# Kernel tuning notes

Measured on AMD Instinct MI355X. Metric: run time of the kernel, lower is better.

Reference implementation:

```python
import jax, jax.numpy as jnp
import numpy as np

N = 20000   # nodes
E = 40000   # directed edges
F_IN = 13   # dataset.num_features
G = 1000    # graphs in batch
DIMS = [(13, 32), (32, 64), (64, 64)]  # (M_in, M_out) per NNConv layer


def setup_inputs() -> dict:
    key = jax.random.key(0)
    ks = list(jax.random.split(key, 32))
    inp = {}
    inp["x"] = jax.random.normal(ks[0], (N, F_IN), jnp.float32)
    inp["edge_index"] = jax.random.randint(ks[1], (2, E), 0, N, dtype=jnp.int32)
    inp["edge_attr"] = jax.random.uniform(ks[2], (E, 5), dtype=jnp.float32)
    inp["batch"] = jnp.sort(jax.random.randint(ks[3], (N,), 0, G, dtype=jnp.int32))
    i = 4
    for l, (mi, mo) in enumerate(DIMS):
        inp[f"w1_{l}"] = jax.random.normal(ks[i], (5, 128), jnp.float32) / np.sqrt(5.0).astype(np.float32); i += 1
        inp[f"b1_{l}"] = jnp.zeros((128,), jnp.float32)
        inp[f"w2_{l}"] = jax.random.normal(ks[i], (128, mi * mo), jnp.float32) / np.sqrt(128.0).astype(np.float32); i += 1
        inp[f"b2_{l}"] = jnp.zeros((mi * mo,), jnp.float32)
        inp[f"root_{l}"] = jax.random.normal(ks[i], (mi, mo), jnp.float32) / np.sqrt(float(mi)).astype(np.float32); i += 1
        inp[f"bias_{l}"] = jnp.zeros((mo,), jnp.float32)
    inp["fc1_w"] = jax.random.normal(ks[i], (64, 32), jnp.float32) / 8.0; i += 1
    inp["fc1_b"] = jnp.zeros((32,), jnp.float32)
    inp["fc2_w"] = jax.random.normal(ks[i], (32, 16), jnp.float32) / np.sqrt(32.0).astype(np.float32); i += 1
    inp["fc2_b"] = jnp.zeros((16,), jnp.float32)
    inp["fc3_w"] = jax.random.normal(ks[i], (16, 1), jnp.float32) / 4.0; i += 1
    inp["fc3_b"] = jnp.zeros((1,), jnp.float32)
    return inp


def _nnconv(x, src, dst, edge_attr, w1, b1, w2, b2, root, bias, mi, mo):
    # edge MLP: [E,5] -> [E,128] -> [E, mi*mo] per-edge weight matrices
    h = jax.nn.relu(edge_attr @ w1 + b1)
    We = (h @ w2 + b2).reshape(-1, mi, mo)          # [E, mi, mo]
    msg = jnp.einsum('ei,eio->eo', x[src], We)      # gather + per-edge matmul
    agg = jax.ops.segment_sum(msg, dst, num_segments=x.shape[0])  # scatter-add
    return x @ root + agg + bias                    # NNConv root weight + bias


def _forward(x, edge_index, edge_attr, batch, convs, fc1_w, fc1_b, fc2_w, fc2_b, fc3_w, fc3_b):
    src, dst = edge_index[0], edge_index[1]
    for (mi, mo), (w1, b1, w2, b2, root, bias) in zip(DIMS, convs):
        x = jax.nn.elu(_nnconv(x, src, dst, edge_attr, w1, b1, w2, b2, root, bias, mi, mo))
    # scatter_mean pooling over graphs
    sums = jax.ops.segment_sum(x, batch, num_segments=G)
    cnt = jax.ops.segment_sum(jnp.ones((x.shape[0],), x.dtype), batch, num_segments=G)
    xg = sums / jnp.maximum(cnt, 1.0)[:, None]
    xg = jax.nn.elu(xg @ fc1_w + fc1_b)
    xg = jax.nn.elu(xg @ fc2_w + fc2_b)
    return (xg @ fc3_w + fc3_b).reshape(-1)


def reference(x, edge_index, edge_attr, batch,
              w1_0, b1_0, w2_0, b2_0, root_0, bias_0,
              w1_1, b1_1, w2_1, b2_1, root_1, bias_1,
              w1_2, b1_2, w2_2, b2_2, root_2, bias_2,
              fc1_w, fc1_b, fc2_w, fc2_b, fc3_w, fc3_b):
    convs = [(w1_0, b1_0, w2_0, b2_0, root_0, bias_0),
             (w1_1, b1_1, w2_1, b2_1, root_1, bias_1),
             (w1_2, b1_2, w2_2, b2_2, root_2, bias_2)]
    return _forward(x, edge_index, edge_attr, batch, convs,
                    fc1_w, fc1_b, fc2_w, fc2_b, fc3_w, fc3_b)
```

## Files before the change

### kernel.cpp

```cpp
#include <hip/hip_runtime.h>
#include <stdint.h>
#include <math.h>

typedef _Float16 half8_t __attribute__((ext_vector_type(8)));
typedef float floatx4 __attribute__((ext_vector_type(4)));

#define NN 20000
#define NE 40000
#define NG 1000
#define NBLK 313
#define NSPLIT 4

__global__ __launch_bounds__(256) void prep_fused_kernel(
    const float* __restrict__ x, _Float16* __restrict__ e16,
    const float* __restrict__ w2a, const float* __restrict__ b2a, _Float16* __restrict__ oa,
    const float* __restrict__ w2b, const float* __restrict__ b2b, _Float16* __restrict__ ob,
    const float* __restrict__ w2c, const float* __restrict__ b2c, _Float16* __restrict__ oc,
    int* __restrict__ deg)
{
  if (blockIdx.x < 1250) {
    int idx = blockIdx.x * 256 + threadIdx.x;
    int n = idx >> 4, i = idx & 15;
    e16[idx] = (i < 13) ? (_Float16)x[(size_t)n * 13 + i] : (_Float16)0.f;
    return;
  }
  if (blockIdx.x >= 1680) {
    int n = (blockIdx.x - 1680) * 256 + threadIdx.x;
    if (n < NN) deg[n] = 0;
    return;
  }
  const int TOT0 = 68 * 2 * 64, TOT1 = 132 * 4 * 64, TOT2 = 264 * 4 * 64;
  int idx = (blockIdx.x - 1250) * 256 + threadIdx.x;
  const float *w2, *b2; _Float16* op; int mi, mo, mpsh, CT;
  if (idx < TOT0) { w2 = w2a; b2 = b2a; op = oa; mi = 13; mo = 32; mpsh = 4; CT = 2; }
  else if (idx < TOT0 + TOT1) { idx -= TOT0; w2 = w2b; b2 = b2b; op = ob; mi = 32; mo = 64; mpsh = 5; CT = 4; }
  else if (idx < TOT0 + TOT1 + TOT2) { idx -= TOT0 + TOT1; w2 = w2c; b2 = b2c; op = oc; mi = 64; mo = 64; mpsh = 6; CT = 4; }
  else return;
  int l = idx & 63;
  int ct = (idx >> 6) % CT;
  int c = idx / (64 * CT);
  int q = l >> 4;
  int n = ct * 16 + (l & 15);
  int mask = (1 << mpsh) - 1;
  half8_t v;
#pragma unroll
  for (int j = 0; j < 8; ++j) {
    int r = c * 32 + q * 8 + j;
    int k = r >> mpsh, i = r & mask;
    float f = 0.f;
    if (i < mi) {
      if (k < 128) f = w2[(size_t)(k * mi + i) * mo + n];
      else if (k == 128) f = b2[(size_t)i * mo + n];
    }
    v[j] = (_Float16)f;
  }
  *(half8_t*)(op + (size_t)idx * 8) = v;
}

__global__ __launch_bounds__(256) void deg_kernel(const int* __restrict__ dst, int* __restrict__ deg) {
  int e = blockIdx.x * 256 + threadIdx.x;
  if (e < NE) atomicAdd(&deg[dst[e]], 1);
}

__global__ __launch_bounds__(1024) void scan_kernel(
    const int* __restrict__ deg, int* __restrict__ row_ptr, int* __restrict__ cursor)
{
  constexpr int CH = 20;
  __shared__ int wsum[16];
  int t = threadIdx.x;
  int lane = t & 63, w = t >> 6;
  int base = t * CH;
  int local[CH];
#pragma unroll
  for (int i = 0; i < CH; ++i) {
    int n = base + i;
    local[i] = (n < NN) ? deg[n] : 0;
  }
  int s = 0;
#pragma unroll
  for (int i = 0; i < CH; ++i) s += local[i];
  int sc = s;
#pragma unroll
  for (int d = 1; d < 64; d <<= 1) {
    int v = __shfl_up(sc, d, 64);
    if (lane >= d) sc += v;
  }
  if (lane == 63) wsum[w] = sc;
  __syncthreads();
  if (w == 0 && lane < 16) {
    int v = wsum[lane];
    int scc = v;
#pragma unroll
    for (int d = 1; d < 16; d <<= 1) {
      int u = __shfl_up(scc, d, 64);
      if (lane >= d) scc += u;
    }
    wsum[lane] = scc - v;
  }
  __syncthreads();
  int run = wsum[w] + (sc - s);
#pragma unroll
  for (int i = 0; i < CH; ++i) {
    int n = base + i;
    if (n < NN) { row_ptr[n] = run; cursor[n] = run; run += local[i]; }
    else if (n == NN) row_ptr[NN] = run;
  }
}

__global__ __launch_bounds__(256) void fill_kernel(
    const int* __restrict__ dst, int* __restrict__ cursor, int* __restrict__ eids)
{
  int e = blockIdx.x * 256 + threadIdx.x;
  if (e < NE) { int p = atomicAdd(&cursor[dst[e]], 1); eids[p] = e; }
}

template <int MIP, int MO, int NCC, int KCNT>
__global__ __launch_bounds__(256, 4) void msg9_kernel(
    const float* __restrict__ ea, const float* __restrict__ w1,
    const float* __restrict__ b1, const _Float16* __restrict__ xe,
    const int* __restrict__ src,
    const _Float16* __restrict__ w2h, _Float16* __restrict__ msgp)
{
  constexpr int EPB = 128;
  constexpr int CT = MO / 16;
  constexpr int CHB = CT * 1024;
  constexpr int XV = (MIP == 64) ? 2 : 1;
  constexpr int KH = (KCNT + 1) >> 1;

  __shared__ uint4 wsb[2][CHB / 16];
  __shared__ _Float16 h16[KCNT * EPB];
  __shared__ float w1s[5 * 128 + 128];

  const int t = threadIdx.x;
  const int wave = t >> 6, lane = t & 63;
  const int l15 = lane & 15, q = lane >> 4;
  const int split = blockIdx.x / NBLK;
  const int e0 = (blockIdx.x % NBLK) * EPB;
  const int c0 = NCC * split;
  const int kg0 = KCNT * split;

  const char* wgp = (const char*)w2h + (size_t)c0 * CHB;
  uint4 ra4, rb4; uint2 ra2, rb2;
  if constexpr (CT == 4) {
    ra4 = *(const uint4*)(wgp + t * 16);
    rb4 = *(const uint4*)(wgp + CHB + t * 16);
  } else {
    ra2 = *(const uint2*)(wgp + t * 8);
    rb2 = *(const uint2*)(wgp + CHB + t * 8);
  }

  const int wbase = wave * 32;
  half8_t xf[2][XV];
#pragma unroll
  for (int s = 0; s < 2; ++s) {
    int eg = e0 + wbase + s * 16 + l15; if (eg >= NE) eg = NE - 1;
    const _Float16* xr = xe + (size_t)src[eg] * MIP;
    int i0 = (MIP == 16) ? (q & 1) * 8 : q * 8;
    xf[s][0] = *(const half8_t*)(xr + i0);
    if constexpr (MIP == 64)
      xf[s][XV - 1] = *(const half8_t*)(xr + 32 + q * 8);
  }

  const int te = t & 127;
  float ear[5];
  {
    int eg = e0 + te; if (eg >= NE) eg = NE - 1;
#pragma unroll
    for (int j = 0; j < 5; ++j) ear[j] = ea[(size_t)eg * 5 + j];
  }
  for (int i = t; i < 768; i += 256) w1s[i] = (i < 640) ? w1[i] : b1[i - 640];
  __syncthreads();

  {
    int kh = t >> 7;
    int klo = kh * KH;
    int khi = klo + KH; if (khi > KCNT) khi = KCNT;
    for (int kl = klo; kl < khi; ++kl) {
      int kg = kg0 + kl;
      float v;
      if (kg < 128) {
        v = w1s[640 + kg];
#pragma unroll
        for (int j = 0; j < 5; ++j) v = fmaf(ear[j], w1s[j * 128 + kg], v);
        v = fmaxf(v, 0.f);
      } else v = (kg == 128) ? 1.f : 0.f;
      h16[kl * EPB + te] = (_Float16)v;
    }
  }
  __syncthreads();

  floatx4 acc[2][CT];
#pragma unroll
  for (int s = 0; s < 2; ++s)
#pragma unroll
    for (int b = 0; b < CT; ++b) acc[s][b] = (floatx4){0.f, 0.f, 0.f, 0.f};

#pragma unroll 2
  for (int cc = 0; cc < NCC; ++cc) {
    const bool odd = (cc & 1) != 0;
    if constexpr (CT == 4) wsb[cc & 1][t] = odd ? rb4 : ra4;
    else ((uint2*)wsb[cc & 1])[t] = odd ? rb2 : ra2;
    if (cc + 2 < NCC) {
      const char* np = wgp + (size_t)(cc + 2) * CHB;
      if constexpr (CT == 4) {
        if (odd) rb4 = *(const uint4*)(np + t * 16); else ra4 = *(const uint4*)(np + t * 16);
      } else {
        if (odd) rb2 = *(const uint2*)(np + t * 8); else ra2 = *(const uint2*)(np + t * 8);
      }
    }
    __syncthreads();
    const _Float16* wb = (const _Float16*)wsb[cc & 1];
    half8_t bf[CT];
#pragma unroll
    for (int b = 0; b < CT; ++b)
      bf[b] = *(const half8_t*)(wb + (b * 64 + lane) * 8);
    int kl;
    if constexpr (MIP == 64) kl = cc >> 1;
    else if constexpr (MIP == 32) kl = cc;
    else kl = 2 * cc + (q >> 1);
#pragma unroll
    for (int s = 0; s < 2; ++s) {
      _Float16 hv = h16[kl * EPB + wbase + s * 16 + l15];
      half8_t af;
      if constexpr (MIP == 64) af = xf[s][cc & 1] * hv;
      else af = xf[s][0] * hv;
#pragma unroll
      for (int b = 0; b < CT; ++b)
        acc[s][b] = __builtin_amdgcn_mfma_f32_16x16x32_f16(af, bf[b], acc[s][b], 0, 0, 0);
    }
  }

  _Float16* mp = msgp + (size_t)split * NE * MO;
#pragma unroll
  for (int s = 0; s < 2; ++s) {
    int rowb = wbase + s * 16 + q * 4;
#pragma unroll
    for (int b = 0; b < CT; ++b) {
      int n = b * 16 + l15;
#pragma unroll
      for (int r = 0; r < 4; ++r) {
        int row = rowb + r;
        int e = e0 + row;
        if (e < NE) mp[(size_t)e * MO + n] = (_Float16)acc[s][b][r];
      }
    }
  }
}

template <int MIP, int NCC, int KCNT>
__global__ __launch_bounds__(256, 4) void msgH_kernel(
    const float* __restrict__ ea, const float* __restrict__ w1,
    const float* __restrict__ b1, const _Float16* __restrict__ xe,
    const int* __restrict__ src,
    const _Float16* __restrict__ w2h, _Float16* __restrict__ msgp)
{
  constexpr int EPB = 128;
  constexpr int MO = 64;
  constexpr int CHB = 4096;
  constexpr int XV = (MIP == 64) ? 2 : 1;
  constexpr int KH = (KCNT + 1) >> 1;

  __shared__ uint4 wsb[2][CHB / 16];
  __shared__ _Float16 h16[KCNT * EPB];
  __shared__ float w1s[5 * 128 + 128];

  const int t = threadIdx.x;
  const int wave = t >> 6, lane = t & 63;
  const int l15 = lane & 15, q = lane >> 4;
  const int mw = wave >> 1;
  const int nw = wave & 1;
  const int split = blockIdx.x / NBLK;
  const int e0 = (blockIdx.x % NBLK) * EPB;
  const int c0 = NCC * split;
  const int kg0 = KCNT * split;

  const char* wgp = (const char*)w2h + (size_t)c0 * CHB;
  uint4 ra4 = *(const uint4*)(wgp + t * 16);
  uint4 rb4 = *(const uint4*)(wgp + CHB + t * 16);

  half8_t xf[4][XV];
#pragma unroll
  for (int s = 0; s < 4; ++s) {
    int eg = e0 + mw * 64 + s * 16 + l15; if (eg >= NE) eg = NE - 1;
    const _Float16* xr = xe + (size_t)src[eg] * MIP;
    xf[s][0] = *(const half8_t*)(xr + q * 8);
    if constexpr (MIP == 64)
      xf[s][XV - 1] = *(const half8_t*)(xr + 32 + q * 8);
  }

  const int te = t & 127;
  float ear[5];
  {
    int eg = e0 + te; if (eg >= NE) eg = NE - 1;
#pragma unroll
    for (int j = 0; j < 5; ++j) ear[j] = ea[(size_t)eg * 5 + j];
  }
  for (int i = t; i < 768; i += 256) w1s[i] = (i < 640) ? w1[i] : b1[i - 640];
  __syncthreads();

  {
    int kh = t >> 7;
    int klo = kh * KH;
    int khi = klo + KH; if (khi > KCNT) khi = KCNT;
    for (int kl = klo; kl < khi; ++kl) {
      int kg = kg0 + kl;
      float v;
      if (kg < 128) {
        v = w1s[640 + kg];
#pragma unroll
        for (int j = 0; j < 5; ++j) v = fmaf(ear[j], w1s[j * 128 + kg], v);
        v = fmaxf(v, 0.f);
      } else v = (kg == 128) ? 1.f : 0.f;
      h16[kl * EPB + te] = (_Float16)v;
    }
  }
  __syncthreads();

  floatx4 acc[4][2];
#pragma unroll
  for (int s = 0; s < 4; ++s)
#pragma unroll
    for (int b = 0; b < 2; ++b) acc[s][b] = (floatx4){0.f, 0.f, 0.f, 0.f};

#pragma unroll 2
  for (int cc = 0; cc < NCC; ++cc) {
    const bool odd = (cc & 1) != 0;
    wsb[cc & 1][t] = odd ? rb4 : ra4;
    if (cc + 2 < NCC) {
      const char* np = wgp + (size_t)(cc + 2) * CHB;
      if (odd) rb4 = *(const uint4*)(np + t * 16); else ra4 = *(const uint4*)(np + t * 16);
    }
    __syncthreads();
    const _Float16* wb = (const _Float16*)wsb[cc & 1];
    half8_t bf[2];
#pragma unroll
    for (int b = 0; b < 2; ++b)
      bf[b] = *(const half8_t*)(wb + ((nw * 2 + b) * 64 + lane) * 8);
    int kl;
    if constexpr (MIP == 64) kl = cc >> 1;
    else kl = cc;
#pragma unroll
    for (int s = 0; s < 4; ++s) {
      _Float16 hv = h16[kl * EPB + mw * 64 + s * 16 + l15];
      half8_t af;
      if constexpr (MIP == 64) af = xf[s][cc & 1] * hv;
      else af = xf[s][0] * hv;
#pragma unroll
      for (int b = 0; b < 2; ++b)
        acc[s][b] = __builtin_amdgcn_mfma_f32_16x16x32_f16(af, bf[b], acc[s][b], 0, 0, 0);
    }
  }

  _Float16* mp = msgp + (size_t)split * NE * MO;
#pragma unroll
  for (int s = 0; s < 4; ++s) {
    int rowb = mw * 64 + s * 16 + q * 4;
#pragma unroll
    for (int b = 0; b < 2; ++b) {
      int n = nw * 32 + b * 16 + l15;
#pragma unroll
      for (int r = 0; r < 4; ++r) {
        int e = e0 + rowb + r;
        if (e < NE) mp[(size_t)e * MO + n] = (_Float16)acc[s][b][r];
      }
    }
  }
}

template <int MIN_, int XST, int MO, int FINAL>
__global__ __launch_bounds__(256) void gather_kernel(
    const _Float16* __restrict__ e16in, const float* __restrict__ root,
    const float* __restrict__ bias, const int* __restrict__ row_ptr,
    const int* __restrict__ eids, const _Float16* __restrict__ msgp,
    _Float16* __restrict__ oute, float* __restrict__ outf)
{
  constexpr int NPB = 256 / MO;
  int n = blockIdx.x * NPB + threadIdx.x / MO;
  int o = threadIdx.x % MO;
  if (n >= NN) return;
  float a = bias[o];
#pragma unroll
  for (int i = 0; i < MIN_; ++i)
    a = fmaf((float)e16in[(size_t)n * XST + i], root[i * MO + o], a);
  int r0 = row_ptr[n], r1 = row_ptr[n + 1];
  for (int j = r0; j < r1; ++j) {
    int e = eids[j];
#pragma unroll
    for (int s = 0; s < NSPLIT; ++s)
      a += (float)msgp[((size_t)s * NE + e) * MO + o];
  }
  if constexpr (FINAL) {
    outf[(size_t)n * MO + o] = a;
  } else {
    float v = a > 0.f ? a : (expf(a) - 1.f);
    oute[(size_t)n * MO + o] = (_Float16)v;
  }
}

__global__ __launch_bounds__(64) void pool_fc_kernel(
    const float* __restrict__ xn2, const int* __restrict__ batch,
    const float* __restrict__ f1w, const float* __restrict__ f1b,
    const float* __restrict__ f2w, const float* __restrict__ f2b,
    const float* __restrict__ f3w, const float* __restrict__ f3b,
    float* __restrict__ out)
{
  __shared__ float xg[64]; __shared__ float a1[32]; __shared__ float a2[16];
  int g = blockIdx.x, t = threadIdx.x;
  int lo = 0, hi = NN;
  while (lo < hi) { int m = (lo + hi) >> 1; if (batch[m] < g) lo = m + 1; else hi = m; }
  int start = lo; hi = NN;
  while (lo < hi) { int m = (lo + hi) >> 1; if (batch[m] <= g) lo = m + 1; else hi = m; }
  int end = lo;
  float acc = 0.f;
  for (int n = start; n < end; ++n) {
    float v = xn2[(size_t)n * 64 + t];
    acc += v > 0.f ? v : (expf(v) - 1.f);
  }
  float c = (end > start) ? (float)(end - start) : 1.f;
  xg[t] = acc / c;
  __syncthreads();
  if (t < 32) {
    float a = f1b[t];
    for (int i = 0; i < 64; ++i) a = fmaf(xg[i], f1w[i * 32 + t], a);
    a1[t] = a > 0.f ? a : (expf(a) - 1.f);
  }
  __syncthreads();
  if (t < 16) {
    float a = f2b[t];
    for (int i = 0; i < 32; ++i) a = fmaf(a1[i], f2w[i * 16 + t], a);
    a2[t] = a > 0.f ? a : (expf(a) - 1.f);
  }
  __syncthreads();
  if (t == 0) {
    float a = f3b[0];
    for (int i = 0; i < 16; ++i) a = fmaf(a2[i], f3w[i], a);
    out[g] = a;
  }
}

extern "C" void kernel_launch(void* const* d_in, const int* in_sizes, int n_in,
                              void* d_out, int out_size, void* d_ws, size_t ws_size,
                              hipStream_t stream)
{
  const float* x_in  = (const float*)d_in[0];
  const int*   ei    = (const int*)d_in[1];
  const float* ea    = (const float*)d_in[2];
  const int*   batch = (const int*)d_in[3];
  const float* W1[3] = {(const float*)d_in[4],  (const float*)d_in[10], (const float*)d_in[16]};
  const float* B1[3] = {(const float*)d_in[5],  (const float*)d_in[11], (const float*)d_in[17]};
  const float* W2[3] = {(const float*)d_in[6],  (const float*)d_in[12], (const float*)d_in[18]};
  const float* B2[3] = {(const float*)d_in[7],  (const float*)d_in[13], (const float*)d_in[19]};
  const float* RT[3] = {(const float*)d_in[8],  (const float*)d_in[14], (const float*)d_in[20]};
  const float* BS[3] = {(const float*)d_in[9],  (const float*)d_in[15], (const float*)d_in[21]};
  const float* f1w = (const float*)d_in[22]; const float* f1b = (const float*)d_in[23];
  const float* f2w = (const float*)d_in[24]; const float* f2b = (const float*)d_in[25];
  const float* f3w = (const float*)d_in[26]; const float* f3b = (const float*)d_in[27];

  char* ws = (char*)d_ws;
  size_t off = 0;
  auto alloc = [&](size_t bytes) { void* p = ws + off; off += (bytes + 255) & ~(size_t)255; return p; };
  float*    xn2   = (float*)alloc((size_t)NN * 64 * 4);
  _Float16* e16_0 = (_Float16*)alloc((size_t)NN * 16 * 2);
  _Float16* e16_1 = (_Float16*)alloc((size_t)NN * 32 * 2);
  _Float16* e16_2 = (_Float16*)alloc((size_t)NN * 64 * 2);
  _Float16* w2h0  = (_Float16*)alloc((size_t)68 * 2048);
  _Float16* w2h1  = (_Float16*)alloc((size_t)132 * 4096);
  _Float16* w2h2  = (_Float16*)alloc((size_t)264 * 4096);
  _Float16* msgp  = (_Float16*)alloc((size_t)NSPLIT * NE * 64 * 2);
  int*      deg     = (int*)alloc((size_t)NN * 4);
  int*      row_ptr = (int*)alloc((size_t)(NN + 1) * 4);
  int*      cursor  = (int*)alloc((size_t)NN * 4);
  int*      eids    = (int*)alloc((size_t)NE * 4);

  const int* srcp = ei;
  const int* dstp = ei + NE;

  prep_fused_kernel<<<1680 + (NN + 255) / 256, 256, 0, stream>>>(
      x_in, e16_0, W2[0], B2[0], w2h0, W2[1], B2[1], w2h1, W2[2], B2[2], w2h2, deg);
  deg_kernel<<<(NE + 255) / 256, 256, 0, stream>>>(dstp, deg);
  scan_kernel<<<1, 1024, 0, stream>>>(deg, row_ptr, cursor);
  fill_kernel<<<(NE + 255) / 256, 256, 0, stream>>>(dstp, cursor, eids);

  msg9_kernel<16, 32, 17, 34><<<NBLK * NSPLIT, 256, 0, stream>>>(
      ea, W1[0], B1[0], e16_0, srcp, w2h0, msgp);
  gather_kernel<13, 16, 32, 0><<<(NN + 7) / 8, 256, 0, stream>>>(
      e16_0, RT[0], BS[0], row_ptr, eids, msgp, e16_1, xn2);

  msgH_kernel<32, 33, 33><<<NBLK * NSPLIT, 256, 0, stream>>>(
      ea, W1[1], B1[1], e16_1, srcp, w2h1, msgp);
  gather_kernel<32, 32, 64, 0><<<(NN + 3) / 4, 256, 0, stream>>>(
      e16_1, RT[1], BS[1], row_ptr, eids, msgp, e16_2, xn2);

  msgH_kernel<64, 66, 33><<<NBLK * NSPLIT, 256, 0, stream>>>(
      ea, W1[2], B1[2], e16_2, srcp, w2h2, msgp);
  gather_kernel<64, 64, 64, 1><<<(NN + 3) / 4, 256, 0, stream>>>(
      e16_2, RT[2], BS[2], row_ptr, eids, msgp, e16_2, xn2);

  pool_fc_kernel<<<NG, 64, 0, stream>>>(xn2, batch, f1w, f1b, f2w, f2b, f3w, f3b, (float*)d_out);
}
```

Before: 297.5 us.

## Process weight chunks in pairs per barrier and give each wave all output columns

```diff
diff --git a/kernel.cpp b/kernel.cpp
--- a/kernel.cpp
+++ b/kernel.cpp
@@ -24,12 +24,12 @@
     e16[idx] = (i < 13) ? (_Float16)x[(size_t)n * 13 + i] : (_Float16)0.f;
     return;
   }
-  if (blockIdx.x >= 1680) {
-    int n = (blockIdx.x - 1680) * 256 + threadIdx.x;
+  if (blockIdx.x >= 1684) {
+    int n = (blockIdx.x - 1684) * 256 + threadIdx.x;
     if (n < NN) deg[n] = 0;
     return;
   }
-  const int TOT0 = 68 * 2 * 64, TOT1 = 132 * 4 * 64, TOT2 = 264 * 4 * 64;
+  const int TOT0 = 68 * 2 * 64, TOT1 = 136 * 4 * 64, TOT2 = 264 * 4 * 64;
   int idx = (blockIdx.x - 1250) * 256 + threadIdx.x;
   const float *w2, *b2; _Float16* op; int mi, mo, mpsh, CT;
   if (idx < TOT0) { w2 = w2a; b2 = b2a; op = oa; mi = 13; mo = 32; mpsh = 4; CT = 2; }
@@ -248,7 +248,7 @@
 }
 
 template <int MIP, int NCC, int KCNT>
-__global__ __launch_bounds__(256, 4) void msgH_kernel(
+__global__ __launch_bounds__(256, 4) void msg9p_kernel(
     const float* __restrict__ ea, const float* __restrict__ w1,
     const float* __restrict__ b1, const _Float16* __restrict__ xe,
     const int* __restrict__ src,
@@ -256,32 +256,35 @@
 {
   constexpr int EPB = 128;
   constexpr int MO = 64;
+  constexpr int CT = 4;
   constexpr int CHB = 4096;
   constexpr int XV = (MIP == 64) ? 2 : 1;
   constexpr int KH = (KCNT + 1) >> 1;
-
-  __shared__ uint4 wsb[2][CHB / 16];
+  static_assert((NCC & 1) == 0, "NCC must be even for paired chunks");
+
+  __shared__ uint4 wsb[2][2][CHB / 16];
   __shared__ _Float16 h16[KCNT * EPB];
   __shared__ float w1s[5 * 128 + 128];
 
   const int t = threadIdx.x;
   const int wave = t >> 6, lane = t & 63;
   const int l15 = lane & 15, q = lane >> 4;
-  const int mw = wave >> 1;
-  const int nw = wave & 1;
   const int split = blockIdx.x / NBLK;
   const int e0 = (blockIdx.x % NBLK) * EPB;
   const int c0 = NCC * split;
   const int kg0 = KCNT * split;
 
   const char* wgp = (const char*)w2h + (size_t)c0 * CHB;
-  uint4 ra4 = *(const uint4*)(wgp + t * 16);
-  uint4 rb4 = *(const uint4*)(wgp + CHB + t * 16);
-
-  half8_t xf[4][XV];
-#pragma unroll
-  for (int s = 0; s < 4; ++s) {
-    int eg = e0 + mw * 64 + s * 16 + l15; if (eg >= NE) eg = NE - 1;
+  uint4 pA0 = *(const uint4*)(wgp + 0 * CHB + t * 16);
+  uint4 pA1 = *(const uint4*)(wgp + 1 * CHB + t * 16);
+  uint4 pB0 = *(const uint4*)(wgp + 2 * CHB + t * 16);
+  uint4 pB1 = *(const uint4*)(wgp + 3 * CHB + t * 16);
+
+  const int wbase = wave * 32;
+  half8_t xf[2][XV];
+#pragma unroll
+  for (int s = 0; s < 2; ++s) {
+    int eg = e0 + wbase + s * 16 + l15; if (eg >= NE) eg = NE - 1;
     const _Float16* xr = xe + (size_t)src[eg] * MIP;
     xf[s][0] = *(const half8_t*)(xr + q * 8);
     if constexpr (MIP == 64)
@@ -316,51 +319,61 @@
   }
   __syncthreads();
 
-  floatx4 acc[4][2];
-#pragma unroll
-  for (int s = 0; s < 4; ++s)
-#pragma unroll
-    for (int b = 0; b < 2; ++b) acc[s][b] = (floatx4){0.f, 0.f, 0.f, 0.f};
+  floatx4 acc[2][CT];
+#pragma unroll
+  for (int s = 0; s < 2; ++s)
+#pragma unroll
+    for (int b = 0; b < CT; ++b) acc[s][b] = (floatx4){0.f, 0.f, 0.f, 0.f};
 
 #pragma unroll 2
-  for (int cc = 0; cc < NCC; ++cc) {
-    const bool odd = (cc & 1) != 0;
-    wsb[cc & 1][t] = odd ? rb4 : ra4;
-    if (cc + 2 < NCC) {
-      const char* np = wgp + (size_t)(cc + 2) * CHB;
-      if (odd) rb4 = *(const uint4*)(np + t * 16); else ra4 = *(const uint4*)(np + t * 16);
+  for (int ci = 0; ci < NCC / 2; ++ci) {
+    const bool odd = (ci & 1) != 0;
+    wsb[ci & 1][0][t] = odd ? pB0 : pA0;
+    wsb[ci & 1][1][t] = odd ? pB1 : pA1;
+    if (2 * ci + 4 < NCC) {
+      const char* np = wgp + (size_t)(2 * ci + 4) * CHB;
+      if (odd) pB0 = *(const uint4*)(np + t * 16); else pA0 = *(const uint4*)(np + t * 16);
+    }
+    if (2 * ci + 5 < NCC) {
+      const char* np = wgp + (size_t)(2 * ci + 5) * CHB;
+      if (odd) pB1 = *(const uint4*)(np + t * 16); else pA1 = *(const uint4*)(np + t * 16);
     }
     __syncthreads();
-    const _Float16* wb = (const _Float16*)wsb[cc & 1];
-    half8_t bf[2];
-#pragma unroll
-    for (int b = 0; b < 2; ++b)
-      bf[b] = *(const half8_t*)(wb + ((nw * 2 + b) * 64 + lane) * 8);
-    int kl;
-    if constexpr (MIP == 64) kl = cc >> 1;
-    else kl = cc;
-#pragma unroll
-    for (int s = 0; s < 4; ++s) {
-      _Float16 hv = h16[kl * EPB + mw * 64 + s * 16 + l15];
-      half8_t af;
-      if constexpr (MIP == 64) af = xf[s][cc & 1] * hv;
-      else af = xf[s][0] * hv;
-#pragma unroll
-      for (int b = 0; b < 2; ++b)
-        acc[s][b] = __builtin_amdgcn_mfma_f32_16x16x32_f16(af, bf[b], acc[s][b], 0, 0, 0);
+#pragma unroll
+    for (int u = 0; u < 2; ++u) {
+      const int cc = 2 * ci + u;
+      const _Float16* wbu = (const _Float16*)wsb[ci & 1][u];
+      half8_t bf[CT];
+#pragma unroll
+      for (int b = 0; b < CT; ++b)
+        bf[b] = *(const half8_t*)(wbu + (b * 64 + lane) * 8);
+      int kl;
+      if constexpr (MIP == 64) kl = cc >> 1;
+      else kl = cc;
+#pragma unroll
+      for (int s = 0; s < 2; ++s) {
+        _Float16 hv = h16[kl * EPB + wbase + s * 16 + l15];
+        half8_t af;
+        if constexpr (MIP == 64) af = xf[s][cc & 1] * hv;
+        else af = xf[s][0] * hv;
+#pragma unroll
+        for (int b = 0; b < CT; ++b)
+          acc[s][b] = __builtin_amdgcn_mfma_f32_16x16x32_f16(af, bf[b], acc[s][b], 0, 0, 0);
+      }
     }
   }
 
   _Float16* mp = msgp + (size_t)split * NE * MO;
 #pragma unroll
-  for (int s = 0; s < 4; ++s) {
-    int rowb = mw * 64 + s * 16 + q * 4;
-#pragma unroll
-    for (int b = 0; b < 2; ++b) {
-      int n = nw * 32 + b * 16 + l15;
+  for (int s = 0; s < 2; ++s) {
+    int rowb = wbase + s * 16 + q * 4;
+#pragma unroll
+    for (int b = 0; b < CT; ++b) {
+      int n = b * 16 + l15;
 #pragma unroll
       for (int r = 0; r < 4; ++r) {
-        int e = e0 + rowb + r;
+        int row = rowb + r;
+        int e = e0 + row;
         if (e < NE) mp[(size_t)e * MO + n] = (_Float16)acc[s][b][r];
       }
     }
@@ -464,7 +477,7 @@
   _Float16* e16_1 = (_Float16*)alloc((size_t)NN * 32 * 2);
   _Float16* e16_2 = (_Float16*)alloc((size_t)NN * 64 * 2);
   _Float16* w2h0  = (_Float16*)alloc((size_t)68 * 2048);
-  _Float16* w2h1  = (_Float16*)alloc((size_t)132 * 4096);
+  _Float16* w2h1  = (_Float16*)alloc((size_t)136 * 4096);
   _Float16* w2h2  = (_Float16*)alloc((size_t)264 * 4096);
   _Float16* msgp  = (_Float16*)alloc((size_t)NSPLIT * NE * 64 * 2);
   int*      deg     = (int*)alloc((size_t)NN * 4);
@@ -475,7 +488,7 @@
   const int* srcp = ei;
   const int* dstp = ei + NE;
 
-  prep_fused_kernel<<<1680 + (NN + 255) / 256, 256, 0, stream>>>(
+  prep_fused_kernel<<<1684 + (NN + 255) / 256, 256, 0, stream>>>(
       x_in, e16_0, W2[0], B2[0], w2h0, W2[1], B2[1], w2h1, W2[2], B2[2], w2h2, deg);
   deg_kernel<<<(NE + 255) / 256, 256, 0, stream>>>(dstp, deg);
   scan_kernel<<<1, 1024, 0, stream>>>(deg, row_ptr, cursor);
@@ -486,12 +499,12 @@
   gather_kernel<13, 16, 32, 0><<<(NN + 7) / 8, 256, 0, stream>>>(
       e16_0, RT[0], BS[0], row_ptr, eids, msgp, e16_1, xn2);
 
-  msgH_kernel<32, 33, 33><<<NBLK * NSPLIT, 256, 0, stream>>>(
+  msg9p_kernel<32, 34, 34><<<NBLK * NSPLIT, 256, 0, stream>>>(
       ea, W1[1], B1[1], e16_1, srcp, w2h1, msgp);
   gather_kernel<32, 32, 64, 0><<<(NN + 3) / 4, 256, 0, stream>>>(
       e16_1, RT[1], BS[1], row_ptr, eids, msgp, e16_2, xn2);
 
-  msgH_kernel<64, 66, 33><<<NBLK * NSPLIT, 256, 0, stream>>>(
+  msg9p_kernel<64, 66, 33><<<NBLK * NSPLIT, 256, 0, stream>>>(
       ea, W1[2], B1[2], e16_2, srcp, w2h2, msgp);
   gather_kernel<64, 64, 64, 1><<<(NN + 3) / 4, 256, 0, stream>>>(
       e16_2, RT[2], BS[2], row_ptr, eids, msgp, e16_2, xn2);
```

Result: no change. 296.2 us (-0.4%).
